# Kernel tuning notes

Measured on AMD Instinct MI355X. Metric: run time of the kernel, lower is better.

The kernel has to match this reference:

```python
import jax, jax.numpy as jnp
import numpy as np

N_NODES = 50000
N_EDGES = 400000
D_NODE = 256
D_EDGE = 64
LN_EPS = 1e-6  # flax LayerNorm default


def _layer_norm(x, scale, bias):
    mu = jnp.mean(x, axis=-1, keepdims=True)
    var = jnp.mean(jnp.square(x - mu), axis=-1, keepdims=True)
    return (x - mu) * jax.lax.rsqrt(var + LN_EPS) * scale + bias


def _glorot(key, shape):
    fan_in, fan_out = shape
    std = jnp.sqrt(2.0 / (fan_in + fan_out))
    return std * jax.random.normal(key, shape, dtype=jnp.float32)


def setup_inputs() -> dict:
    key = jax.random.key(0)
    ks = jax.random.split(key, 10)
    inp = {
        "nodes": jax.random.normal(ks[0], (N_NODES, D_NODE), dtype=jnp.float32),
        "edges": jax.random.normal(ks[1], (N_EDGES, D_EDGE), dtype=jnp.float32),
        "senders": jax.random.randint(ks[2], (N_EDGES,), 0, N_NODES, dtype=jnp.int32),
        "receivers": jax.random.randint(ks[3], (N_EDGES,), 0, N_NODES, dtype=jnp.int32),
        # message projection (no bias)
        "W_message": _glorot(ks[4], (D_NODE + D_EDGE, D_NODE)),
        # NodeMLP (ReluMLP_skip) with n_features_list_nodes = [256, 256, 256]
        "mlp_W0": _glorot(ks[5], (D_NODE, D_NODE)), "mlp_b0": jnp.zeros((D_NODE,), jnp.float32),
        "mlp_W1": _glorot(ks[6], (D_NODE, D_NODE)), "mlp_b1": jnp.zeros((D_NODE,), jnp.float32),
        "mlp_W2": _glorot(ks[7], (D_NODE, D_NODE)), "mlp_b2": jnp.zeros((D_NODE,), jnp.float32),
        # LayerNorm params
        "ln_aggr_scale": jnp.ones((D_NODE,), jnp.float32), "ln_aggr_bias": jnp.zeros((D_NODE,), jnp.float32),
        "ln_out_scale": jnp.ones((D_NODE,), jnp.float32), "ln_out_bias": jnp.zeros((D_NODE,), jnp.float32),
    }
    return inp


def _relu_mlp_skip(x, Ws, bs):
    # Dense layers; ReLU on all but the last; residual add whenever widths match.
    n = len(Ws)
    for i, (W, b) in enumerate(zip(Ws, bs)):
        y = x @ W + b
        if i < n - 1:
            y = jax.nn.relu(y)
        x = x + y if y.shape[-1] == x.shape[-1] else y
    return x


def reference(nodes, edges, senders, receivers, W_message,
              mlp_W0, mlp_b0, mlp_W1, mlp_b1, mlp_W2, mlp_b2,
              ln_aggr_scale, ln_aggr_bias, ln_out_scale, ln_out_bias):
    total_nodes = nodes.shape[0]
    sender_features = nodes[senders]                      # [E, d] gather
    msg_in = jnp.concatenate([sender_features, edges], axis=-1)  # [E, d+d_e]
    messages = msg_in @ W_message                          # [E, d]
    agg = jax.ops.segment_sum(messages, receivers, num_segments=total_nodes)  # [N, d]
    h = _layer_norm(jax.nn.relu(agg) + nodes, ln_aggr_scale, ln_aggr_bias)
    nodes_out = _relu_mlp_skip(h, [mlp_W0, mlp_W1, mlp_W2], [mlp_b0, mlp_b1, mlp_b2])
    nodes_new = _layer_norm(nodes + nodes_out, ln_out_scale, ln_out_bias)
    return nodes_new
```

## Files before the change

### kernel.cpp

```cpp
#include <hip/hip_runtime.h>

#define NN 50000
#define NE 400000

typedef unsigned short u16;
typedef unsigned int   u32;
typedef __bf16 bf16x4 __attribute__((ext_vector_type(4)));
typedef __bf16 bf16x8 __attribute__((ext_vector_type(8)));
typedef float  f32x4  __attribute__((ext_vector_type(4)));

union ABFrag { bf16x8 v; bf16x4 h[2]; };
union BFrag  { uint4 u; bf16x8 v; };

__device__ __forceinline__ u16 f2bfu(float f) {
  u32 u = __builtin_bit_cast(u32, f);
  return (u16)((u + 0x7FFFu + ((u >> 16) & 1u)) >> 16);
}
__device__ __forceinline__ float bf2f(u16 u) {
  return __builtin_bit_cast(float, (u32)u << 16);
}

__global__ __launch_bounds__(256) void k_cvt(const float* __restrict__ src,
                                             u16* __restrict__ dst, int n4) {
  int i = blockIdx.x * 256 + threadIdx.x;
  if (i >= n4) return;
  float4 f = ((const float4*)src)[i];
  ushort4 o;
  o.x = f2bfu(f.x); o.y = f2bfu(f.y); o.z = f2bfu(f.z); o.w = f2bfu(f.w);
  ((ushort4*)dst)[i] = o;
}

__device__ __forceinline__ void pack_one(const float* __restrict__ W,
                                         u16* __restrict__ P, int idx) {
  int k = idx >> 8, n = idx & 255;
  int t = k >> 5, kp = k & 31;
  int g = (kp & 15) >> 2;
  int j = (kp & 3) | ((kp >> 4) << 2);
  P[(((t << 8) + n) << 5) + (g << 3) + j] = f2bfu(W[idx]);
}

__global__ __launch_bounds__(256) void k_pack4(
    const float* __restrict__ Wm, const float* __restrict__ W0,
    const float* __restrict__ W1, const float* __restrict__ W2,
    u16* __restrict__ Pm, u16* __restrict__ P0,
    u16* __restrict__ P1, u16* __restrict__ P2) {
  int idx = blockIdx.x * 256 + threadIdx.x;
  const int S0 = 320 * 256, S1 = S0 + 256 * 256, S2 = S1 + 256 * 256, S3 = S2 + 256 * 256;
  if (idx < S0)      pack_one(Wm, Pm, idx);
  else if (idx < S1) pack_one(W0, P0, idx - S0);
  else if (idx < S2) pack_one(W1, P1, idx - S1);
  else if (idx < S3) pack_one(W2, P2, idx - S2);
}

__global__ __launch_bounds__(256) void k_hist(const int* __restrict__ recv,
                                              int* __restrict__ cnt) {
  int i = blockIdx.x * 256 + threadIdx.x;
  if (i < NE) atomicAdd(&cnt[recv[i]], 1);
}

__global__ __launch_bounds__(256) void k_scan1(const int* __restrict__ cnt,
                                               int* __restrict__ loc,
                                               int* __restrict__ bsum) {
  __shared__ int sm[256];
  int t = threadIdx.x, i = blockIdx.x * 256 + t;
  int v = (i < NN) ? cnt[i] : 0;
  sm[t] = v;
  __syncthreads();
  #pragma unroll
  for (int d = 1; d < 256; d <<= 1) {
    int x = sm[t];
    int y = (t >= d) ? sm[t - d] : 0;
    __syncthreads();
    sm[t] = x + y;
    __syncthreads();
  }
  if (i < NN) loc[i] = sm[t] - v;
  if (t == 255) bsum[blockIdx.x] = sm[255];
}

__global__ __launch_bounds__(256) void k_scan2(int* __restrict__ bsum,
                                               int* __restrict__ bpre, int nb) {
  __shared__ int sm[256];
  int t = threadIdx.x;
  int v = (t < nb) ? bsum[t] : 0;
  sm[t] = v;
  __syncthreads();
  #pragma unroll
  for (int d = 1; d < 256; d <<= 1) {
    int x = sm[t];
    int y = (t >= d) ? sm[t - d] : 0;
    __syncthreads();
    sm[t] = x + y;
    __syncthreads();
  }
  if (t < nb) bpre[t] = sm[t] - v;
}

__global__ __launch_bounds__(256) void k_scan3(const int* __restrict__ loc,
                                               const int* __restrict__ bpre,
                                               int* __restrict__ offs,
                                               int* __restrict__ cursor) {
  int i = blockIdx.x * 256 + threadIdx.x;
  if (i < NN) {
    int o = loc[i] + bpre[blockIdx.x];
    offs[i] = o;
    cursor[i] = o;
  }
  if (i == NN - 1) offs[NN] = NE;
}

__global__ __launch_bounds__(256) void k_scatter(
    const int* __restrict__ snd, const int* __restrict__ recv,
    int* __restrict__ cursor, int* __restrict__ s_snd, int* __restrict__ s_eid) {
  int e = blockIdx.x * 256 + threadIdx.x;
  if (e < NE) {
    int p = atomicAdd(&cursor[recv[e]], 1);
    s_snd[p] = snd[e];
    s_eid[p] = e;
  }
}

__global__ __launch_bounds__(256) void k_aggr(
    const u16* __restrict__ nodes_bf, const float* __restrict__ edges,
    const int* __restrict__ offs, const int* __restrict__ s_snd,
    const int* __restrict__ s_eid, u16* __restrict__ X)
{
  const int wid = blockIdx.x * 4 + (threadIdx.x >> 6);
  const int lane = threadIdx.x & 63;
  const int beg = offs[wid], end = offs[wid + 1];
  float a0 = 0.f, a1 = 0.f, a2 = 0.f, a3 = 0.f, a4 = 0.f;
  int j = beg;
  for (; j + 1 < end; j += 2) {
    int sA = s_snd[j],     eA = s_eid[j];
    int sB = s_snd[j + 1], eB = s_eid[j + 1];
    ushort4 nA = *(const ushort4*)(nodes_bf + (size_t)sA * 256 + lane * 4);
    ushort4 nB = *(const ushort4*)(nodes_bf + (size_t)sB * 256 + lane * 4);
    float evA = edges[(size_t)eA * 64 + lane];
    float evB = edges[(size_t)eB * 64 + lane];
    a0 += bf2f(nA.x) + bf2f(nB.x); a1 += bf2f(nA.y) + bf2f(nB.y);
    a2 += bf2f(nA.z) + bf2f(nB.z); a3 += bf2f(nA.w) + bf2f(nB.w);
    a4 += evA + evB;
  }
  if (j < end) {
    int sA = s_snd[j], eA = s_eid[j];
    ushort4 nA = *(const ushort4*)(nodes_bf + (size_t)sA * 256 + lane * 4);
    a0 += bf2f(nA.x); a1 += bf2f(nA.y); a2 += bf2f(nA.z); a3 += bf2f(nA.w);
    a4 += edges[(size_t)eA * 64 + lane];
  }
  u16* xr = X + (size_t)wid * 320;
  ushort4 o;
  o.x = f2bfu(a0); o.y = f2bfu(a1); o.z = f2bfu(a2); o.w = f2bfu(a3);
  *(ushort4*)(xr + lane * 4) = o;
  xr[256 + lane] = f2bfu(a4);
}


#define AT_ADDR(r, c) (atb + ((((r) * 640) + ((c) * 2)) ^ (((r) & 7) << 4)))

#define WRBT(c, v) do { int _c = (c); \
  int _i = (((_c >> 10) << 13) + ((_c & 3) << 11) + (((_c & 1023) >> 2) << 3)) ^ ((_c & 3) << 4); \
  *(uint4*)&Bt[_i] = (v); } while (0)

#define MFMA_STEP(t) \
  _Pragma("unroll") \
  for (int kk = 0; kk < 2; ++kk) { \
    ABFrag a; \
    const int kc = (((t) * 2 + kk) << 5) + (g << 2); \
    const int m = wr16 + l16; \
    a.h[0] = *(const bf16x4*)AT_ADDR(m, kc); \
    a.h[1] = *(const bf16x4*)AT_ADDR(m, kc + 16); \
    _Pragma("unroll") \
    for (int q = 0; q < 4; ++q) { \
      BFrag b; \
      b.u = *(const uint4*)&Bt[((kk << 13) + (g << 11) + ((wcn + (q << 4) + l16) << 3)) ^ (g << 4)]; \
      acc[q] = __builtin_amdgcn_mfma_f32_16x16x32_bf16(a.v, b.v, acc[q], 0, 0, 0); \
    } \
  }

#define RUN_LAYER(wp, T) do { \
  const u16* pb = (wp) + ((size_t)tid << 3); \
  uint4 p0 = *(const uint4*)(pb); \
  uint4 p1 = *(const uint4*)(pb + 8192); \
  _Pragma("unroll 1") \
  for (int t = 0; t < (T); ++t) { \
    __syncthreads(); \
    WRBT(tid, p0); WRBT(tid + 1024, p1); \
    if (t + 1 < (T)) { \
      const u16* nb = pb + ((size_t)(t + 1) << 14); \
      p0 = *(const uint4*)nb; p1 = *(const uint4*)(nb + 8192); \
    } \
    __syncthreads(); \
    MFMA_STEP(t) \
  } \
} while (0)

#define LN_STATS() do { \
  _Pragma("unroll") \
  for (int r = 0; r < 4; ++r) { \
    float s  = acc[0][r] + acc[1][r] + acc[2][r] + acc[3][r]; \
    float s2 = acc[0][r]*acc[0][r] + acc[1][r]*acc[1][r] + acc[2][r]*acc[2][r] + acc[3][r]*acc[3][r]; \
    s  += __shfl_xor(s, 1);  s  += __shfl_xor(s, 2);  s  += __shfl_xor(s, 4);  s  += __shfl_xor(s, 8); \
    s2 += __shfl_xor(s2, 1); s2 += __shfl_xor(s2, 2); s2 += __shfl_xor(s2, 4); s2 += __shfl_xor(s2, 8); \
    if (l16 == 0) { int m = wr16 + g4 + r; red[m][wc2] = s; red[m][wc2 + 1] = s2; } \
  } \
  __syncthreads(); \
  if (tid < 64) { \
    float s  = red[tid][0] + red[tid][2] + red[tid][4] + red[tid][6]; \
    float s2 = red[tid][1] + red[tid][3] + red[tid][5] + red[tid][7]; \
    float mu  = s * (1.f / 256.f); \
    float var = s2 * (1.f / 256.f) - mu * mu; \
    murs[tid][0] = mu; murs[tid][1] = rsqrtf(var + 1e-6f); \
  } \
  __syncthreads(); \
} while (0)

__global__ __launch_bounds__(1024)
void k_fused(
    const u16* __restrict__ X, const float* __restrict__ nodes,
    const u16* __restrict__ wm, const u16* __restrict__ w0,
    const u16* __restrict__ w1, const u16* __restrict__ w2,
    const float* __restrict__ b0, const float* __restrict__ b1,
    const float* __restrict__ b2,
    const float* __restrict__ lnAs, const float* __restrict__ lnAb,
    const float* __restrict__ lnOs, const float* __restrict__ lnOb,
    float* __restrict__ out)
{
  __shared__ u16 At[64 * 320];
  __shared__ u16 Bt[16384];
  __shared__ float red[64][8];
  __shared__ float murs[64][2];

  const int tid = threadIdx.x;
  const int lane = tid & 63;
  const int w16 = tid >> 6;
  const int wr16 = (w16 >> 2) << 4;
  const int wcn = (w16 & 3) << 6;
  const int wc2 = (w16 & 3) << 1;
  const int l16 = lane & 15, g = lane >> 4, g4 = g << 2;
  const int r0 = blockIdx.x * 64;

  char* const atb = (char*)At;

  #pragma unroll
  for (int it = 0; it < 3; ++it) {
    int c = tid + it * 1024;
    if (c < 2560) {
      int r = c / 40, seg = c - r * 40;
      int row = r0 + r;
      uint4 v = {0u, 0u, 0u, 0u};
      if (row < NN) v = *(const uint4*)(X + (size_t)row * 320 + seg * 8);
      *(uint4*)(atb + ((r * 640 + seg * 16) ^ ((r & 7) << 4))) = v;
    }
  }

  f32x4 acc[4];
  const f32x4 z = {0.f, 0.f, 0.f, 0.f};
  #pragma unroll
  for (int q = 0; q < 4; ++q) acc[q] = z;

  RUN_LAYER(wm, 5);

  #pragma unroll
  for (int q = 0; q < 4; ++q) {
    int n = wcn + (q << 4) + l16;
    #pragma unroll
    for (int r = 0; r < 4; ++r) {
      int row = r0 + wr16 + g4 + r;
      float nv = (row < NN) ? nodes[(size_t)row * 256 + n] : 0.f;
      acc[q][r] = fmaxf(acc[q][r], 0.f) + nv;
    }
  }
  LN_STATS();
  #pragma unroll
  for (int q = 0; q < 4; ++q) {
    int n = wcn + (q << 4) + l16;
    float scl = lnAs[n], bia = lnAb[n];
    #pragma unroll
    for (int r = 0; r < 4; ++r) {
      int m = wr16 + g4 + r;
      float h = (acc[q][r] - murs[m][0]) * murs[m][1] * scl + bia;
      *(u16*)AT_ADDR(m, n) = f2bfu(h);
      acc[q][r] = 0.f;
    }
  }

  #pragma unroll 1
  for (int l = 0; l < 3; ++l) {
    const u16* wp = (l == 0) ? w0 : (l == 1) ? w1 : w2;
    RUN_LAYER(wp, 4);
    __syncthreads();

    if (l < 2) {
      const float* bp = (l == 0) ? b0 : b1;
      #pragma unroll
      for (int q = 0; q < 4; ++q) {
        int n = wcn + (q << 4) + l16;
        float bn = bp[n];
        #pragma unroll
        for (int r = 0; r < 4; ++r) {
          int m = wr16 + g4 + r;
          u16* p = (u16*)AT_ADDR(m, n);
          float xn = bf2f(*p) + fmaxf(acc[q][r] + bn, 0.f);
          *p = f2bfu(xn);
          acc[q][r] = 0.f;
        }
      }
    } else {
      #pragma unroll
      for (int q = 0; q < 4; ++q) {
        int n = wcn + (q << 4) + l16;
        float bn = b2[n];
        #pragma unroll
        for (int r = 0; r < 4; ++r) {
          int m = wr16 + g4 + r;
          int row = r0 + m;
          float nv = (row < NN) ? nodes[(size_t)row * 256 + n] : 0.f;
          acc[q][r] = nv + bf2f(*(const u16*)AT_ADDR(m, n)) + acc[q][r] + bn;
        }
      }
    }
  }

  LN_STATS();
  #pragma unroll
  for (int q = 0; q < 4; ++q) {
    int n = wcn + (q << 4) + l16;
    float scl = lnOs[n], bia = lnOb[n];
    #pragma unroll
    for (int r = 0; r < 4; ++r) {
      int m = wr16 + g4 + r;
      int row = r0 + m;
      if (row < NN)
        out[(size_t)row * 256 + n] =
            (acc[q][r] - murs[m][0]) * murs[m][1] * scl + bia;
    }
  }
}

extern "C" void kernel_launch(void* const* d_in, const int* in_sizes, int n_in,
                              void* d_out, int out_size, void* d_ws, size_t ws_size,
                              hipStream_t stream)
{
  const float* nodes = (const float*)d_in[0];
  const float* edges = (const float*)d_in[1];
  const int* senders = (const int*)d_in[2];
  const int* receivers = (const int*)d_in[3];
  const float* Wmsg = (const float*)d_in[4];
  const float* W0 = (const float*)d_in[5];
  const float* b0 = (const float*)d_in[6];
  const float* W1 = (const float*)d_in[7];
  const float* b1 = (const float*)d_in[8];
  const float* W2 = (const float*)d_in[9];
  const float* b2 = (const float*)d_in[10];
  const float* lnAs = (const float*)d_in[11];
  const float* lnAb = (const float*)d_in[12];
  const float* lnOs = (const float*)d_in[13];
  const float* lnOb = (const float*)d_in[14];
  float* out = (float*)d_out;
  (void)in_sizes; (void)n_in; (void)out_size; (void)ws_size;

  char* w = (char*)d_ws;
  size_t off = 0;
  auto take = [&](size_t b) { void* p = w + off; off += (b + 511) & ~(size_t)511; return p; };

  u16*   nodes_bf = (u16*)take((size_t)NN * 256 * 2);
  u16*   wmsg_p   = (u16*)take(320 * 256 * 2);
  u16*   w0_p     = (u16*)take(256 * 256 * 2);
  u16*   w1_p     = (u16*)take(256 * 256 * 2);
  u16*   w2_p     = (u16*)take(256 * 256 * 2);
  u16*   X        = (u16*)take((size_t)NN * 320 * 2);
  int*   cnt      = (int*)take((size_t)NN * 4);
  int*   loc      = (int*)take((size_t)NN * 4);
  int*   offs     = (int*)take((size_t)(NN + 1) * 4);
  int*   cursor   = (int*)take((size_t)NN * 4);
  int*   s_snd    = (int*)take((size_t)NE * 4);
  int*   s_eid    = (int*)take((size_t)NE * 4);
  int*   bsum     = (int*)take(256 * 4);
  int*   bpre     = (int*)take(256 * 4);

  const int NB = (NN + 255) / 256;

  hipMemsetAsync(cnt, 0, (size_t)NN * 4, stream);
  k_cvt<<<(NN * 256 / 4 + 255) / 256, 256, 0, stream>>>(nodes, nodes_bf, NN * 256 / 4);
  k_pack4<<<(320 * 256 + 3 * 256 * 256) / 256, 256, 0, stream>>>(
      Wmsg, W0, W1, W2, wmsg_p, w0_p, w1_p, w2_p);

  k_hist<<<(NE + 255) / 256, 256, 0, stream>>>(receivers, cnt);
  k_scan1<<<NB, 256, 0, stream>>>(cnt, loc, bsum);
  k_scan2<<<1, 256, 0, stream>>>(bsum, bpre, NB);
  k_scan3<<<NB, 256, 0, stream>>>(loc, bpre, offs, cursor);
  k_scatter<<<(NE + 255) / 256, 256, 0, stream>>>(senders, receivers, cursor, s_snd, s_eid);

  k_aggr<<<NN / 4, 256, 0, stream>>>(nodes_bf, edges, offs, s_snd, s_eid, X);

  const int MB = (NN + 63) / 64;
  k_fused<<<MB, 1024, 0, stream>>>(X, nodes, wmsg_p, w0_p, w1_p, w2_p,
                                   b0, b1, b2, lnAs, lnAb, lnOs, lnOb, out);
}
```

Baseline: 233.2 us.

## Fuse edge aggregation into MLP kernel and merge prep kernels into one launch

The gather-and-sum over incoming edges now runs inside the fused MLP kernel and writes straight into shared memory, so the intermediate X buffer in global memory and the separate aggregation kernel are gone. Conversion of nodes to bf16, weight packing and the receiver histogram are merged into one launch with block ranges split by role. This removes global write/read traffic and two launches. In exchange, the 1024-thread fused blocks, with few blocks per CU, now run latency-bound gathers before their MFMA work, which may hide gather latency worse than the old lightweight aggregation kernel did.

After: 235.2 us. No clear change (+0.8%).

```diff
diff --git a/kernel.cpp b/kernel.cpp
--- a/kernel.cpp
+++ b/kernel.cpp
@@ -18,16 +18,6 @@
 }
 __device__ __forceinline__ float bf2f(u16 u) {
   return __builtin_bit_cast(float, (u32)u << 16);
-}
-
-__global__ __launch_bounds__(256) void k_cvt(const float* __restrict__ src,
-                                             u16* __restrict__ dst, int n4) {
-  int i = blockIdx.x * 256 + threadIdx.x;
-  if (i >= n4) return;
-  float4 f = ((const float4*)src)[i];
-  ushort4 o;
-  o.x = f2bfu(f.x); o.y = f2bfu(f.y); o.z = f2bfu(f.z); o.w = f2bfu(f.w);
-  ((ushort4*)dst)[i] = o;
 }
 
 __device__ __forceinline__ void pack_one(const float* __restrict__ W,
@@ -39,23 +29,36 @@
   P[(((t << 8) + n) << 5) + (g << 3) + j] = f2bfu(W[idx]);
 }
 
-__global__ __launch_bounds__(256) void k_pack4(
+#define NB_CVT  12500
+#define NB_PACK 1088
+#define NB_HIST 1563
+
+__global__ __launch_bounds__(256) void k_prep(
+    const float* __restrict__ nodes, u16* __restrict__ nodes_bf,
     const float* __restrict__ Wm, const float* __restrict__ W0,
     const float* __restrict__ W1, const float* __restrict__ W2,
     u16* __restrict__ Pm, u16* __restrict__ P0,
-    u16* __restrict__ P1, u16* __restrict__ P2) {
-  int idx = blockIdx.x * 256 + threadIdx.x;
-  const int S0 = 320 * 256, S1 = S0 + 256 * 256, S2 = S1 + 256 * 256, S3 = S2 + 256 * 256;
-  if (idx < S0)      pack_one(Wm, Pm, idx);
-  else if (idx < S1) pack_one(W0, P0, idx - S0);
-  else if (idx < S2) pack_one(W1, P1, idx - S1);
-  else if (idx < S3) pack_one(W2, P2, idx - S2);
-}
-
-__global__ __launch_bounds__(256) void k_hist(const int* __restrict__ recv,
-                                              int* __restrict__ cnt) {
-  int i = blockIdx.x * 256 + threadIdx.x;
-  if (i < NE) atomicAdd(&cnt[recv[i]], 1);
+    u16* __restrict__ P1, u16* __restrict__ P2,
+    const int* __restrict__ recv, int* __restrict__ cnt)
+{
+  int b = blockIdx.x, t = threadIdx.x;
+  if (b < NB_CVT) {
+    int i = b * 256 + t;
+    float4 f = ((const float4*)nodes)[i];
+    ushort4 o;
+    o.x = f2bfu(f.x); o.y = f2bfu(f.y); o.z = f2bfu(f.z); o.w = f2bfu(f.w);
+    ((ushort4*)nodes_bf)[i] = o;
+  } else if (b < NB_CVT + NB_PACK) {
+    int idx = (b - NB_CVT) * 256 + t;
+    const int S0 = 320 * 256, S1 = S0 + 65536, S2 = S1 + 65536;
+    if (idx < S0)      pack_one(Wm, Pm, idx);
+    else if (idx < S1) pack_one(W0, P0, idx - S0);
+    else if (idx < S2) pack_one(W1, P1, idx - S1);
+    else               pack_one(W2, P2, idx - S2);
+  } else {
+    int i = (b - NB_CVT - NB_PACK) * 256 + t;
+    if (i < NE) atomicAdd(&cnt[recv[i]], 1);
+  }
 }
 
 __global__ __launch_bounds__(256) void k_scan1(const int* __restrict__ cnt,
@@ -118,40 +121,6 @@
     s_snd[p] = snd[e];
     s_eid[p] = e;
   }
-}
-
-__global__ __launch_bounds__(256) void k_aggr(
-    const u16* __restrict__ nodes_bf, const float* __restrict__ edges,
-    const int* __restrict__ offs, const int* __restrict__ s_snd,
-    const int* __restrict__ s_eid, u16* __restrict__ X)
-{
-  const int wid = blockIdx.x * 4 + (threadIdx.x >> 6);
-  const int lane = threadIdx.x & 63;
-  const int beg = offs[wid], end = offs[wid + 1];
-  float a0 = 0.f, a1 = 0.f, a2 = 0.f, a3 = 0.f, a4 = 0.f;
-  int j = beg;
-  for (; j + 1 < end; j += 2) {
-    int sA = s_snd[j],     eA = s_eid[j];
-    int sB = s_snd[j + 1], eB = s_eid[j + 1];
-    ushort4 nA = *(const ushort4*)(nodes_bf + (size_t)sA * 256 + lane * 4);
-    ushort4 nB = *(const ushort4*)(nodes_bf + (size_t)sB * 256 + lane * 4);
-    float evA = edges[(size_t)eA * 64 + lane];
-    float evB = edges[(size_t)eB * 64 + lane];
-    a0 += bf2f(nA.x) + bf2f(nB.x); a1 += bf2f(nA.y) + bf2f(nB.y);
-    a2 += bf2f(nA.z) + bf2f(nB.z); a3 += bf2f(nA.w) + bf2f(nB.w);
-    a4 += evA + evB;
-  }
-  if (j < end) {
-    int sA = s_snd[j], eA = s_eid[j];
-    ushort4 nA = *(const ushort4*)(nodes_bf + (size_t)sA * 256 + lane * 4);
-    a0 += bf2f(nA.x); a1 += bf2f(nA.y); a2 += bf2f(nA.z); a3 += bf2f(nA.w);
-    a4 += edges[(size_t)eA * 64 + lane];
-  }
-  u16* xr = X + (size_t)wid * 320;
-  ushort4 o;
-  o.x = f2bfu(a0); o.y = f2bfu(a1); o.z = f2bfu(a2); o.w = f2bfu(a3);
-  *(ushort4*)(xr + lane * 4) = o;
-  xr[256 + lane] = f2bfu(a4);
 }
 
 
@@ -216,7 +185,10 @@
 
 __global__ __launch_bounds__(1024)
 void k_fused(
-    const u16* __restrict__ X, const float* __restrict__ nodes,
+    const u16* __restrict__ nodes_bf, const float* __restrict__ edges,
+    const int* __restrict__ offs, const int* __restrict__ s_snd,
+    const int* __restrict__ s_eid,
+    const float* __restrict__ nodes,
     const u16* __restrict__ wm, const u16* __restrict__ w0,
     const u16* __restrict__ w1, const u16* __restrict__ w2,
     const float* __restrict__ b0, const float* __restrict__ b1,
@@ -241,15 +213,38 @@
 
   char* const atb = (char*)At;
 
-  #pragma unroll
-  for (int it = 0; it < 3; ++it) {
-    int c = tid + it * 1024;
-    if (c < 2560) {
-      int r = c / 40, seg = c - r * 40;
-      int row = r0 + r;
-      uint4 v = {0u, 0u, 0u, 0u};
-      if (row < NN) v = *(const uint4*)(X + (size_t)row * 320 + seg * 8);
-      *(uint4*)(atb + ((r * 640 + seg * 16) ^ ((r & 7) << 4))) = v;
+  {
+    const int m0 = w16 << 2;
+    #pragma unroll 1
+    for (int i = 0; i < 4; ++i) {
+      const int m = m0 + i;
+      const int node = r0 + m;
+      float a0 = 0.f, a1 = 0.f, a2 = 0.f, a3 = 0.f, a4 = 0.f;
+      if (node < NN) {
+        int beg = offs[node], end = offs[node + 1];
+        int j = beg;
+        for (; j + 1 < end; j += 2) {
+          int sA = s_snd[j],     eA = s_eid[j];
+          int sB = s_snd[j + 1], eB = s_eid[j + 1];
+          ushort4 nA = *(const ushort4*)(nodes_bf + (size_t)sA * 256 + (lane << 2));
+          ushort4 nB = *(const ushort4*)(nodes_bf + (size_t)sB * 256 + (lane << 2));
+          float evA = edges[(size_t)eA * 64 + lane];
+          float evB = edges[(size_t)eB * 64 + lane];
+          a0 += bf2f(nA.x) + bf2f(nB.x); a1 += bf2f(nA.y) + bf2f(nB.y);
+          a2 += bf2f(nA.z) + bf2f(nB.z); a3 += bf2f(nA.w) + bf2f(nB.w);
+          a4 += evA + evB;
+        }
+        if (j < end) {
+          int sA = s_snd[j], eA = s_eid[j];
+          ushort4 nA = *(const ushort4*)(nodes_bf + (size_t)sA * 256 + (lane << 2));
+          a0 += bf2f(nA.x); a1 += bf2f(nA.y); a2 += bf2f(nA.z); a3 += bf2f(nA.w);
+          a4 += edges[(size_t)eA * 64 + lane];
+        }
+      }
+      ushort4 o;
+      o.x = f2bfu(a0); o.y = f2bfu(a1); o.z = f2bfu(a2); o.w = f2bfu(a3);
+      *(ushort4*)AT_ADDR(m, lane << 2) = o;
+      *(u16*)AT_ADDR(m, 256 + lane) = f2bfu(a4);
     }
   }
 
@@ -368,7 +363,6 @@
   u16*   w0_p     = (u16*)take(256 * 256 * 2);
   u16*   w1_p     = (u16*)take(256 * 256 * 2);
   u16*   w2_p     = (u16*)take(256 * 256 * 2);
-  u16*   X        = (u16*)take((size_t)NN * 320 * 2);
   int*   cnt      = (int*)take((size_t)NN * 4);
   int*   loc      = (int*)take((size_t)NN * 4);
   int*   offs     = (int*)take((size_t)(NN + 1) * 4);
@@ -381,19 +375,17 @@
   const int NB = (NN + 255) / 256;
 
   hipMemsetAsync(cnt, 0, (size_t)NN * 4, stream);
-  k_cvt<<<(NN * 256 / 4 + 255) / 256, 256, 0, stream>>>(nodes, nodes_bf, NN * 256 / 4);
-  k_pack4<<<(320 * 256 + 3 * 256 * 256) / 256, 256, 0, stream>>>(
-      Wmsg, W0, W1, W2, wmsg_p, w0_p, w1_p, w2_p);
-
-  k_hist<<<(NE + 255) / 256, 256, 0, stream>>>(receivers, cnt);
+  k_prep<<<NB_CVT + NB_PACK + NB_HIST, 256, 0, stream>>>(
+      nodes, nodes_bf, Wmsg, W0, W1, W2, wmsg_p, w0_p, w1_p, w2_p,
+      receivers, cnt);
+
   k_scan1<<<NB, 256, 0, stream>>>(cnt, loc, bsum);
   k_scan2<<<1, 256, 0, stream>>>(bsum, bpre, NB);
   k_scan3<<<NB, 256, 0, stream>>>(loc, bpre, offs, cursor);
   k_scatter<<<(NE + 255) / 256, 256, 0, stream>>>(senders, receivers, cursor, s_snd, s_eid);
 
-  k_aggr<<<NN / 4, 256, 0, stream>>>(nodes_bf, edges, offs, s_snd, s_eid, X);
-
   const int MB = (NN + 63) / 64;
-  k_fused<<<MB, 1024, 0, stream>>>(X, nodes, wmsg_p, w0_p, w1_p, w2_p,
+  k_fused<<<MB, 1024, 0, stream>>>(nodes_bf, edges, offs, s_snd, s_eid,
+                                   nodes, wmsg_p, w0_p, w1_p, w2_p,
                                    b0, b1, b2, lnAs, lnAb, lnOs, lnOb, out);
 }
```
